# Kernel tuning notes

Measured on AMD Instinct MI355X. Metric: run time of the kernel, lower is better.

Reference implementation:

```python
import jax, jax.numpy as jnp
import numpy as np

B, L, E = 64, 256, 512
H = 1024          # hidden_size
N = 128           # memory_size
HS = 64           # head_size (memory width)
NH = 4            # NTM heads
OUT = 1024        # output_size
TNH = 4           # transformer nhead
IN_DIM = E + NH * HS          # 768
POD = H + NH * HS             # 1280


def ln(x, g, b, eps=1e-5):
    mu = x.mean(-1, keepdims=True)
    v = ((x - mu) ** 2).mean(-1, keepdims=True)
    return (x - mu) / jnp.sqrt(v + eps) * g + b


def setup_inputs() -> dict:
    key = jax.random.key(0)
    ks = iter(jax.random.split(key, 64))
    def w(shape, s=0.05):
        return jax.random.normal(next(ks), shape, jnp.float32) * s
    f32 = jnp.float32
    return dict(
        x_emb=jax.random.normal(next(ks), (B, L, E), f32),
        in_g=jnp.ones(IN_DIM, f32), in_b=jnp.zeros(IN_DIM, f32),
        W_ih=w((4 * H, IN_DIM)), W_hh=w((4 * H, H)),
        b_ih=jnp.zeros(4 * H, f32), b_hh=jnp.zeros(4 * H, f32),
        cn_g=jnp.ones(H, f32), cn_b=jnp.zeros(H, f32),
        W_rk=w((NH * HS, H)), b_rk=jnp.zeros(NH * HS, f32),
        W_wk=w((NH * HS, H)), b_wk=jnp.zeros(NH * HS, f32),
        W_ws=w((NH, H)), b_ws=jnp.zeros(NH, f32),
        W_ev=w((NH * HS, H)), b_ev=jnp.zeros(NH * HS, f32),
        attn_w=w((3 * HS, HS)), attn_b=jnp.zeros(3 * HS, f32),
        attn_ow=w((HS, HS)), attn_ob=jnp.zeros(HS, f32),
        l1_w=w((2 * HS, HS)), l1_b=jnp.zeros(2 * HS, f32),
        l2_w=w((HS, 2 * HS)), l2_b=jnp.zeros(HS, f32),
        tn1_g=jnp.ones(HS, f32), tn1_b=jnp.zeros(HS, f32),
        tn2_g=jnp.ones(HS, f32), tn2_b=jnp.zeros(HS, f32),
        rkn_g=jnp.ones(HS, f32), rkn_b=jnp.zeros(HS, f32),
        wkn_g=jnp.ones(HS, f32), wkn_b=jnp.zeros(HS, f32),
        mn_g=jnp.ones(HS, f32), mn_b=jnp.zeros(HS, f32),
        po_g=jnp.ones(POD, f32), po_b=jnp.zeros(POD, f32),
        W_proj=w((OUT, POD)), b_proj=jnp.zeros(OUT, f32),
    )


def reference(x_emb, in_g, in_b, W_ih, W_hh, b_ih, b_hh, cn_g, cn_b,
              W_rk, b_rk, W_wk, b_wk, W_ws, b_ws, W_ev, b_ev,
              attn_w, attn_b, attn_ow, attn_ob, l1_w, l1_b, l2_w, l2_b,
              tn1_g, tn1_b, tn2_g, tn2_b, rkn_g, rkn_b, wkn_g, wkn_b,
              mn_g, mn_b, po_g, po_b, W_proj, b_proj):
    Bc = x_emb.shape[0]
    dh = HS // TNH

    def tblock(mem):  # [B, N, HS], eval-mode (dropout = identity)
        qkv = mem @ attn_w.T + attn_b
        q, k, v = jnp.split(qkv, 3, axis=-1)
        q = q.reshape(Bc, N, TNH, dh)
        k = k.reshape(Bc, N, TNH, dh)
        v = v.reshape(Bc, N, TNH, dh)
        a = jax.nn.softmax(jnp.einsum('bqhd,bkhd->bhqk', q, k) / jnp.sqrt(jnp.float32(dh)), axis=-1)
        o = jnp.einsum('bhqk,bkhd->bqhd', a, v).reshape(Bc, N, HS)
        o = o @ attn_ow.T + attn_ob
        x = ln(mem + o, tn1_g, tn1_b)
        ff = jax.nn.gelu(x @ l1_w.T + l1_b, approximate=False) @ l2_w.T + l2_b
        return ln(x + ff, tn2_g, tn2_b)

    def step(carry, x_t):
        h, c, mem, rc = carry
        inp = ln(jnp.concatenate([x_t, rc.reshape(Bc, -1)], axis=-1), in_g, in_b)
        gates = inp @ W_ih.T + b_ih + h @ W_hh.T + b_hh  # torch gate order i,f,g,o
        i, f, g, o = jnp.split(gates, 4, axis=-1)
        c = jax.nn.sigmoid(f) * c + jax.nn.sigmoid(i) * jnp.tanh(g)
        h = jax.nn.sigmoid(o) * jnp.tanh(c)
        hn = ln(h, cn_g, cn_b)
        rk = (hn @ W_rk.T + b_rk).reshape(Bc, NH, HS)
        wk = (hn @ W_wk.T + b_wk).reshape(Bc, NH, HS)
        ws = jax.nn.sigmoid(hn @ W_ws.T + b_ws)                    # [B, NH]
        ev = jax.nn.sigmoid(hn @ W_ev.T + b_ev).reshape(Bc, NH, HS)
        # addressing
        mem = tblock(mem)
        mem_n = ln(mem, mn_g, mn_b)
        rk = ln(rk, rkn_g, rkn_b)
        wk = ln(wk, wkn_g, wkn_b)
        rw = jax.nn.softmax(jnp.einsum('bnk,bmk->bnm', rk, mem_n), axis=-1)
        rc = jnp.einsum('bnm,bmh->bnh', rw, mem)
        ww = jax.nn.softmax(jnp.einsum('bnk,bmk->bnm', wk, mem_n), axis=-1)
        erase = jnp.einsum('bnm,bnh->bmh', ww, ev)
        mem = mem * (1.0 - erase)
        add = jnp.einsum('bnm,bnh->bmh', ww, ws[..., None] * wk)
        mem = mem + add
        out = ln(jnp.concatenate([hn, rc.reshape(Bc, -1)], axis=-1), po_g, po_b)
        logits = out @ W_proj.T + b_proj
        return (h, c, mem, rc), logits

    h0 = jnp.zeros((Bc, H), x_emb.dtype)
    c0 = jnp.zeros((Bc, H), x_emb.dtype)
    mem0 = jnp.zeros((Bc, N, HS), x_emb.dtype)
    rc0 = jnp.zeros((Bc, NH, HS), x_emb.dtype)
    (h, c, mem, _), outs = jax.lax.scan(step, (h0, c0, mem0, rc0), jnp.swapaxes(x_emb, 0, 1))
    return jnp.swapaxes(outs, 0, 1), mem, (h[None], c[None])
```

## Files before the change

### kernel.cpp

```cpp
#include <hip/hip_runtime.h>
#include <math.h>

typedef short s8v __attribute__((ext_vector_type(8)));
typedef float f32x4 __attribute__((ext_vector_type(4)));

__device__ inline float sigm(float x) { return 1.0f / (1.0f + expf(-x)); }
__device__ inline float dot4(const float4 a, const float4 b) {
  return a.x*b.x + a.y*b.y + a.z*b.z + a.w*b.w;
}
__device__ inline float wsum(float v) {
#pragma unroll
  for (int o = 32; o > 0; o >>= 1) v += __shfl_xor(v, o, 64);
  return v;
}
__device__ inline short f2bf(float f) {
  unsigned int u = __float_as_uint(f);
  unsigned int r = u + 0x7FFFu + ((u >> 16) & 1u);
  return (short)(r >> 16);
}
__device__ inline float bf2f(short h) {
  return __uint_as_float(((unsigned int)(unsigned short)h) << 16);
}
__device__ inline void storesplit(float v, short* __restrict__ hi,
                                  short* __restrict__ lo, size_t idx) {
  short h = f2bf(v);
  hi[idx] = h;
  lo[idx] = f2bf(v - bf2f(h));
}

template<int LD, int KS>
__device__ __forceinline__ void gemm4(const short* __restrict__ A,
                                      const short* __restrict__ B,
                                      f32x4 acc[4], int lane) {
  int off = (lane & 15) * LD + ((lane >> 4) * 8);
#pragma unroll 4
  for (int kb = 0; kb < KS; kb++) {
    int ko = off + kb*32;
    s8v bb = *(const s8v*)(B + ko);
#pragma unroll
    for (int m = 0; m < 4; m++) {
      s8v aa = *(const s8v*)(A + ko + m*16*LD);
      acc[m] = __builtin_amdgcn_mfma_f32_16x16x32_bf16(aa, bb, acc[m], 0,0,0);
    }
  }
}

__global__ void kprep_g(const float* __restrict__ Wih, const float* __restrict__ Whh,
                        short* __restrict__ WgH, short* __restrict__ WgL) {
  int r = blockIdx.y, k = blockIdx.x*256 + threadIdx.x;
  if (k < 1792) {
    int jt = r >> 6, rr = r & 63, ul = rr >> 2, gi = rr & 3;
    int orow = gi*1024 + jt*16 + ul;
    float v = (k < 768) ? Wih[(size_t)orow*768 + k] : Whh[(size_t)orow*1024 + (k-768)];
    storesplit(v, WgH, WgL, (size_t)r*1792 + k);
  }
}
__global__ void kprep_p(const float* __restrict__ Wp, short* __restrict__ W) {
  int j = blockIdx.y, k = blockIdx.x*256 + threadIdx.x;
  W[(size_t)j*1280 + k] = f2bf(Wp[(size_t)j*1280 + k]);
}
__global__ void kprep_h(const float* __restrict__ Wrk, const float* __restrict__ Wwk,
                        const float* __restrict__ Wev, const float* __restrict__ Wws,
                        short* __restrict__ WhH, short* __restrict__ WhL) {
  int j = blockIdx.y, k = blockIdx.x*256 + threadIdx.x;
  float v;
  if (j < 256)      v = Wrk[(size_t)j*1024 + k];
  else if (j < 512) v = Wwk[(size_t)(j-256)*1024 + k];
  else if (j < 768) v = Wev[(size_t)(j-512)*1024 + k];
  else if (j < 772) v = Wws[(size_t)(j-768)*1024 + k];
  else v = 0.f;
  storesplit(v, WhH, WhL, (size_t)j*1024 + k);
}
__global__ void kprep_q(const float* __restrict__ aw, short* __restrict__ WH,
                        short* __restrict__ WL) {
  int i = blockIdx.x*64 + threadIdx.x;
  storesplit(aw[i], WH, WL, i);
}

__global__ __launch_bounds__(256) void k_prep0(
    const float* __restrict__ x_emb, const float* __restrict__ in_g,
    const float* __restrict__ in_b, short* __restrict__ inbH,
    short* __restrict__ inbL)
{
  __shared__ float rs[4], rq[4];
  int b = blockIdx.x, tid = threadIdx.x, lane = tid & 63, wid = tid >> 6;
  float v3[3]; float s = 0.f, sq = 0.f;
#pragma unroll
  for (int i = 0; i < 3; i++) {
    int k = tid + i * 256;
    float v = (k < 512) ? x_emb[(size_t)b * 256 * 512 + k] : 0.f;
    v3[i] = v; s += v; sq += v * v;
  }
  s = wsum(s); sq = wsum(sq);
  if (lane == 0) { rs[wid] = s; rq[wid] = sq; }
  __syncthreads();
  float ts = rs[0]+rs[1]+rs[2]+rs[3], tq = rq[0]+rq[1]+rq[2]+rq[3];
  float mu = ts / 768.f, var = tq / 768.f - mu * mu;
  float rstd = rsqrtf(var + 1e-5f);
#pragma unroll
  for (int i = 0; i < 3; i++) {
    int k = tid + i * 256;
    storesplit((v3[i] - mu) * rstd * in_g[k] + in_b[k], inbH, inbL, b*1792 + k);
  }
}

__global__ __launch_bounds__(512) void kAB(
    const short* __restrict__ inbH, const short* __restrict__ inbL,
    short* __restrict__ inbHn, short* __restrict__ inbLn,
    const short* __restrict__ WgH, const short* __restrict__ WgL,
    const float* __restrict__ b_ih, const float* __restrict__ b_hh,
    float* __restrict__ cbuf, float* __restrict__ hbuf,
    float* __restrict__ hstat, unsigned* __restrict__ gctr,
    const short* __restrict__ membH, const short* __restrict__ membL,
    const short* __restrict__ WqH, const short* __restrict__ WqL,
    const float* __restrict__ attn_b,
    float* __restrict__ mem,
    const float* __restrict__ attn_ow, const float* __restrict__ attn_ob,
    const float* __restrict__ l1w, const float* __restrict__ l1b,
    const float* __restrict__ l2w, const float* __restrict__ l2b,
    const float* __restrict__ tn1g, const float* __restrict__ tn1b,
    const float* __restrict__ tn2g, const float* __restrict__ tn2b,
    const float* __restrict__ cn_g, const float* __restrict__ cn_b,
    const short* __restrict__ WhH, const short* __restrict__ WhL,
    float* __restrict__ hp,
    const short* __restrict__ pob16, const short* __restrict__ Wp16,
    const float* __restrict__ b_proj, float* __restrict__ outs, int t)
{
  __shared__ float pool[35200];
  int bid = blockIdx.x, tid = threadIdx.x, lane = tid & 63;
  if (bid < 64) {
    if (t >= 256) return;
    int jt = bid;
    int kt = tid >> 8;
    int tl = tid & 255;
    int w4 = (tid >> 6) & 3;
    short (*sT)[4][2560] = (short(*)[4][2560])((char*)pool + kt*40960);
    int k0 = kt * 896;
    int srow = tl >> 2, scol = (tl & 3) * 8;
    const short* gAH = inbH + srow*1792 + k0 + scol;
    const short* gAL = inbL + srow*1792 + k0 + scol;
    const short* gBH = WgH + (size_t)(jt*64 + srow)*1792 + k0 + scol;
    const short* gBL = WgL + (size_t)(jt*64 + srow)*1792 + k0 + scol;
    int4 rAH = *(const int4*)gAH, rAL = *(const int4*)gAL;
    int4 rBH = *(const int4*)gBH, rBL = *(const int4*)gBL;
    *(int4*)&sT[0][0][srow*40 + scol] = rAH;
    *(int4*)&sT[0][1][srow*40 + scol] = rAL;
    *(int4*)&sT[0][2][srow*40 + scol] = rBH;
    *(int4*)&sT[0][3][srow*40 + scol] = rBL;
    f32x4 acc[4] = {};
    int arow = lane & 15, akk = (lane >> 4) * 8;
    for (int c = 0; c < 28; ++c) {
      int cur = c & 1;
      if (c < 27) {
        rAH = *(const int4*)(gAH + (c+1)*32);
        rAL = *(const int4*)(gAL + (c+1)*32);
        rBH = *(const int4*)(gBH + (c+1)*32);
        rBL = *(const int4*)(gBL + (c+1)*32);
      }
      __syncthreads();
      s8v bh = *(const s8v*)&sT[cur][2][(w4*16 + arow)*40 + akk];
      s8v bl = *(const s8v*)&sT[cur][3][(w4*16 + arow)*40 + akk];
#pragma unroll
      for (int ms = 0; ms < 4; ++ms) {
        s8v ah = *(const s8v*)&sT[cur][0][(arow + ms*16)*40 + akk];
        s8v al = *(const s8v*)&sT[cur][1][(arow + ms*16)*40 + akk];
        acc[ms] = __builtin_amdgcn_mfma_f32_16x16x32_bf16(ah, bh, acc[ms], 0,0,0);
        acc[ms] = __builtin_amdgcn_mfma_f32_16x16x32_bf16(al, bh, acc[ms], 0,0,0);
        acc[ms] = __builtin_amdgcn_mfma_f32_16x16x32_bf16(ah, bl, acc[ms], 0,0,0);
      }
      if (c < 27) {
        *(int4*)&sT[cur^1][0][srow*40 + scol] = rAH;
        *(int4*)&sT[cur^1][1][srow*40 + scol] = rAL;
        *(int4*)&sT[cur^1][2][srow*40 + scol] = rBH;
        *(int4*)&sT[cur^1][3][srow*40 + scol] = rBL;
      }
    }
    __syncthreads();
    float* sC = pool;
    float* sRed = pool + 8704;
    {
      float* sCk = sC + kt*4352;
      int rr = w4*16 + (lane & 15);
#pragma unroll
      for (int ms = 0; ms < 4; ms++)
#pragma unroll
        for (int r = 0; r < 4; r++) {
          int b = ms*16 + (lane>>4)*4 + r;
          sCk[b*68 + rr] = acc[ms][r];
        }
    }
    __syncthreads();
    {
      int b = tid & 63, ug = tid >> 6;
      float sh = 0.f, sh2 = 0.f;
#pragma unroll
      for (int q = 0; q < 2; q++) {
        int ul = ug*2 + q;
        int u = jt*16 + ul;
        float gi_ = sC[b*68 + ul*4 + 0] + sC[4352 + b*68 + ul*4 + 0] + b_ih[u]        + b_hh[u];
        float gf  = sC[b*68 + ul*4 + 1] + sC[4352 + b*68 + ul*4 + 1] + b_ih[1024 + u] + b_hh[1024 + u];
        float gg  = sC[b*68 + ul*4 + 2] + sC[4352 + b*68 + ul*4 + 2] + b_ih[2048 + u] + b_hh[2048 + u];
        float go  = sC[b*68 + ul*4 + 3] + sC[4352 + b*68 + ul*4 + 3] + b_ih[3072 + u] + b_hh[3072 + u];
        float cn = sigm(gf)*cbuf[b*1024 + u] + sigm(gi_)*tanhf(gg);
        float hh = sigm(go)*tanhf(cn);
        cbuf[b*1024 + u] = cn;
        hbuf[b*1024 + u] = hh;
        storesplit(hh, inbHn, inbLn, b*1792 + 768 + u);
        sh += hh; sh2 += hh*hh;
      }
      sRed[ug*64 + b] = sh;
      sRed[512 + ug*64 + b] = sh2;
    }
    __syncthreads();
    if (tid < 64) {
      float s0 = 0.f, s1 = 0.f;
#pragma unroll
      for (int p = 0; p < 8; p++) { s0 += sRed[p*64 + tid]; s1 += sRed[512 + p*64 + tid]; }
      hstat[(tid*64 + jt)*2]     = s0;
      hstat[(tid*64 + jt)*2 + 1] = s1;
    }
    __syncthreads();
    if (tid == 0) {
      __threadfence();
      __hip_atomic_fetch_add(gctr, 1u, __ATOMIC_RELEASE, __HIP_MEMORY_SCOPE_AGENT);
    }
  } else if (bid < 320) {
    if (t >= 256) return;
    float* sK  = pool;
    float* sV  = pool + 8704;
    float* sX  = pool + 17408;
    float* sM  = pool + 19584;
    float* sO  = pool + 21760;
    float* sS  = pool + 23936;
    float* sRed= pool + 34176;
    int pb = bid - 64;
    int b = pb & 63, mt = pb >> 6;
    int m0 = mt * 32;
    int wid = tid >> 6;
    {
      const short* Ah = membH + (size_t)b * 8192;
      const short* Al = membL + (size_t)b * 8192;
      int ao = (wid*16 + (lane & 15)) * 64 + (lane >> 4) * 8;
      s8v ah0 = *(const s8v*)(Ah + ao);
      s8v ah1 = *(const s8v*)(Ah + ao + 32);
      s8v al0 = *(const s8v*)(Al + ao);
      s8v al1 = *(const s8v*)(Al + ao + 32);
      int bo = (lane & 15) * 64 + (lane >> 4) * 8;
      for (int n = 0; n < 12; n++) {
        s8v bh0 = *(const s8v*)(WqH + bo + n*1024);
        s8v bh1 = *(const s8v*)(WqH + bo + n*1024 + 32);
        s8v bl0 = *(const s8v*)(WqL + bo + n*1024);
        s8v bl1 = *(const s8v*)(WqL + bo + n*1024 + 32);
        f32x4 acc = {};
        acc = __builtin_amdgcn_mfma_f32_16x16x32_bf16(ah0, bh0, acc, 0,0,0);
        acc = __builtin_amdgcn_mfma_f32_16x16x32_bf16(ah1, bh1, acc, 0,0,0);
        acc = __builtin_amdgcn_mfma_f32_16x16x32_bf16(al0, bh0, acc, 0,0,0);
        acc = __builtin_amdgcn_mfma_f32_16x16x32_bf16(al1, bh1, acc, 0,0,0);
        acc = __builtin_amdgcn_mfma_f32_16x16x32_bf16(ah0, bl0, acc, 0,0,0);
        acc = __builtin_amdgcn_mfma_f32_16x16x32_bf16(ah1, bl1, acc, 0,0,0);
        int j = n*16 + (lane & 15);
        int ch = j >> 6, jj = j & 63;
        float bv = attn_b[j];
#pragma unroll
        for (int r = 0; r < 4; r++) {
          int mr = wid*16 + (lane>>4)*4 + r;
          float v = acc[r] + bv;
          if (ch == 0) {
            if (mr >= m0 && mr < m0 + 32) sX[(mr - m0)*68 + jj] = v;
          } else if (ch == 1) sK[mr*64 + jj] = v;
          else sV[mr*64 + jj] = v;
        }
      }
    }
    {
      int i = tid*4;
      int m = i >> 6, s = i & 63;
      *(float4*)&sM[m*68+s] = *(const float4*)&mem[(size_t)b*8192 + m0*64 + i];
    }
    __syncthreads();
    int m = tid >> 4, hd = (tid >> 2) & 3, q = tid & 3;
    const float* qp = sX + m*68 + hd*16;
    float4 q0 = *(const float4*)(qp),   q1 = *(const float4*)(qp+4);
    float4 q2 = *(const float4*)(qp+8), q3 = *(const float4*)(qp+12);
    int kmb = q * 32;
    float mx = -1e30f;
#pragma unroll 4
    for (int kk = 0; kk < 32; kk++) {
      const float* kp = sK + (kmb+kk)*64 + hd*16;
      float sc = dot4(q0, *(const float4*)kp)     + dot4(q1, *(const float4*)(kp+4))
               + dot4(q2, *(const float4*)(kp+8)) + dot4(q3, *(const float4*)(kp+12));
      mx = fmaxf(mx, sc * 0.25f);
    }
    float4 o0 = {0,0,0,0}, o1 = {0,0,0,0}, o2 = {0,0,0,0}, o3 = {0,0,0,0};
    float sum = 0.f;
#pragma unroll 4
    for (int kk = 0; kk < 32; kk++) {
      const float* kp = sK + (kmb+kk)*64 + hd*16;
      float sc = dot4(q0, *(const float4*)kp)     + dot4(q1, *(const float4*)(kp+4))
               + dot4(q2, *(const float4*)(kp+8)) + dot4(q3, *(const float4*)(kp+12));
      float e = expf(sc * 0.25f - mx);
      sum += e;
      const float* vp = sV + (kmb+kk)*64 + hd*16;
      float4 v0 = *(const float4*)vp,     v1 = *(const float4*)(vp+4);
      float4 v2 = *(const float4*)(vp+8), v3 = *(const float4*)(vp+12);
      o0.x += e*v0.x; o0.y += e*v0.y; o0.z += e*v0.z; o0.w += e*v0.w;
      o1.x += e*v1.x; o1.y += e*v1.y; o1.z += e*v1.z; o1.w += e*v1.w;
      o2.x += e*v2.x; o2.y += e*v2.y; o2.z += e*v2.z; o2.w += e*v2.w;
      o3.x += e*v3.x; o3.y += e*v3.y; o3.z += e*v3.z; o3.w += e*v3.w;
    }
    {
      float* pp = sS + tid*20;
      *(float4*)&pp[0]  = o0; *(float4*)&pp[4]  = o1;
      *(float4*)&pp[8]  = o2; *(float4*)&pp[12] = o3;
      sRed[tid] = mx; sRed[512+tid] = sum;
    }
    __syncthreads();
    if (q == 0) {
      float m1 = sRed[tid+1], m2 = sRed[tid+2], m3 = sRed[tid+3];
      float M = fmaxf(fmaxf(mx, m1), fmaxf(m2, m3));
      float e0 = expf(mx - M), e1 = expf(m1 - M), e2 = expf(m2 - M), e3 = expf(m3 - M);
      float inv = 1.0f / (sum*e0 + sRed[512+tid+1]*e1 + sRed[512+tid+2]*e2
                          + sRed[512+tid+3]*e3);
      const float* p1 = sS + (tid+1)*20;
      const float* p2 = sS + (tid+2)*20;
      const float* p3 = sS + (tid+3)*20;
      float oo[16];
      *(float4*)&oo[0] = o0; *(float4*)&oo[4] = o1;
      *(float4*)&oo[8] = o2; *(float4*)&oo[12] = o3;
      float* op = sO + m*68 + hd*16;
#pragma unroll
      for (int d = 0; d < 16; d++)
        op[d] = (oo[d]*e0 + p1[d]*e1 + p2[d]*e2 + p3[d]*e3) * inv;
    }
    __syncthreads();
    for (int idx = tid; idx < 4096; idx += 512) {
      int j = idx >> 6, s = idx & 63;
      sS[j*68 + s] = attn_ow[idx];
    }
    __syncthreads();
    {
      int mm = tid >> 4, jset = tid & 15;
      float4 orow[16];
#pragma unroll
      for (int r = 0; r < 16; r++) orow[r] = *(const float4*)&sO[mm*68 + r*4];
#pragma unroll
      for (int i = 0; i < 4; i++) {
        int j = jset + 16*i;
        const float* wr = sS + j*68;
        float acc = attn_ob[j];
#pragma unroll
        for (int r = 0; r < 16; r++) acc += dot4(orow[r], *(const float4*)&wr[r*4]);
        sM[mm*68 + j] += acc;
      }
    }
    __syncthreads();
    for (int r = wid; r < 32; r += 8) {
      float v = sM[r*68 + lane];
      float ssum = wsum(v), ssq = wsum(v*v);
      float mu = ssum*(1.f/64), var = ssq*(1.f/64) - mu*mu;
      sX[r*68+lane] = (v - mu)*rsqrtf(var+1e-5f)*tn1g[lane] + tn1b[lane];
    }
    for (int idx = tid; idx < 8192; idx += 512) {
      int f = idx >> 6, s = idx & 63;
      sK[f*68 + s] = l1w[idx];
    }
    for (int idx = tid; idx < 8192; idx += 512) {
      int j = idx >> 7, s = idx & 127;
      sV[j*132 + s] = l2w[idx];
    }
    __syncthreads();
    {
      int mm = tid >> 4, fs = tid & 15;
      float4 xr[16];
#pragma unroll
      for (int r = 0; r < 16; r++) xr[r] = *(const float4*)&sX[mm*68 + r*4];
#pragma unroll 4
      for (int i = 0; i < 8; i++) {
        int f = fs + 16*i;
        const float* wr = sK + f*68;
        float acc = l1b[f];
#pragma unroll
        for (int r = 0; r < 16; r++) acc += dot4(xr[r], *(const float4*)&wr[r*4]);
        sS[mm*132 + f] = 0.5f*acc*(1.0f + erff(acc*0.70710678118654752f));
      }
    }
    __syncthreads();
    {
      int mm = tid >> 4, jset = tid & 15;
      float acc6[4];
#pragma unroll
      for (int i = 0; i < 4; i++) acc6[i] = sX[mm*68 + jset + 16*i] + l2b[jset + 16*i];
#pragma unroll
      for (int h = 0; h < 2; h++) {
        float4 fr[16];
#pragma unroll
        for (int r = 0; r < 16; r++) fr[r] = *(const float4*)&sS[mm*132 + h*64 + r*4];
#pragma unroll
        for (int i = 0; i < 4; i++) {
          int j = jset + 16*i;
          const float* wr = sV + j*132 + h*64;
          float a = 0.f;
#pragma unroll
          for (int r = 0; r < 16; r++) a += dot4(fr[r], *(const float4*)&wr[r*4]);
          acc6[i] += a;
        }
      }
#pragma unroll
      for (int i = 0; i < 4; i++) sO[mm*68 + jset + 16*i] = acc6[i];
    }
    __syncthreads();
    for (int r = wid; r < 32; r += 8) {
      float v = sO[r*68 + lane];
      float ssum = wsum(v), ssq = wsum(v*v);
      float mu = ssum*(1.f/64), var = ssq*(1.f/64) - mu*mu;
      mem[(size_t)b*8192 + (m0+r)*64 + lane] =
          (v - mu)*rsqrtf(var+1e-5f)*tn2g[lane] + tn2b[lane];
    }
  } else if (bid < 328) {
    if (t == 0) return;
    int jt = bid - 320;
    int w = tid >> 6;
    f32x4 acc[4] = {};
    const short* B = Wp16 + (size_t)(jt*128 + w*16) * 1280;
    gemm4<1280, 40>(pob16, B, acc, lane);
    int j = jt*128 + w*16 + (lane & 15);
    float bv = b_proj[j];
#pragma unroll
    for (int ms = 0; ms < 4; ms++)
#pragma unroll
      for (int r = 0; r < 4; r++) {
        int b = ms*16 + (lane>>4)*4 + r;
        outs[((size_t)b*256 + (t-1))*1024 + j] = acc[ms][r] + bv;
      }
  } else {
    if (t >= 256) return;
    int wid = tid >> 6;
    if (tid == 0) {
      unsigned target = 64u * (unsigned)(t + 1);
      while (__hip_atomic_load(gctr, __ATOMIC_ACQUIRE, __HIP_MEMORY_SCOPE_AGENT) < target)
        __builtin_amdgcn_s_sleep(2);
    }
    __syncthreads();
    int hb = bid - 328;
    int kt = hb & 3, jt = hb >> 2;
    {
      int b2 = tid & 63, part = tid >> 6;
      float s0 = 0.f, s1 = 0.f;
#pragma unroll 4
      for (int m2 = 0; m2 < 8; m2++) {
        int jt2 = part*8 + m2;
        s0 += hstat[(b2*64 + jt2)*2];
        s1 += hstat[(b2*64 + jt2)*2 + 1];
      }
      pool[part*64 + b2] = s0;
      pool[512 + part*64 + b2] = s1;
    }
    __syncthreads();
    if (tid < 64) {
      float ts = 0.f, tq = 0.f;
#pragma unroll
      for (int p2 = 0; p2 < 8; p2++) {
        ts += pool[p2*64 + tid];
        tq += pool[512 + p2*64 + tid];
      }
      float mu = ts / 1024.f;
      pool[1024+tid] = mu;
      pool[1088+tid] = rsqrtf(tq/1024.f - mu*mu + 1e-5f);
    }
    __syncthreads();
    short* sAH = (short*)&pool[1152];
    short* sAL = sAH + 2560;
    int srow = tid >> 3, scol = (tid & 7) * 4;
    int arow = lane & 15, akk = (lane >> 4) * 8;
    f32x4 acc[4] = {};
    for (int c = 0; c < 8; ++c) {
      __syncthreads();
      {
        float mu = pool[1024 + srow], rsd = pool[1088 + srow];
        int kbase = kt*256 + c*32 + scol;
        const float* hpt = hbuf + srow*1024 + kbase;
#pragma unroll
        for (int i = 0; i < 4; i++) {
          float hnv = (hpt[i] - mu) * rsd * cn_g[kbase + i] + cn_b[kbase + i];
          short hh = f2bf(hnv);
          sAH[srow*40 + scol + i] = hh;
          sAL[srow*40 + scol + i] = f2bf(hnv - bf2f(hh));
        }
      }
      __syncthreads();
      if (wid < 4) {
        size_t bo = (size_t)(jt*64 + wid*16 + arow)*1024 + kt*256 + c*32 + akk;
        s8v bh = *(const s8v*)(WhH + bo);
        s8v bl = *(const s8v*)(WhL + bo);
#pragma unroll
        for (int ms = 0; ms < 4; ++ms) {
          s8v ah = *(const s8v*)&sAH[(arow + ms*16)*40 + akk];
          s8v al = *(const s8v*)&sAL[(arow + ms*16)*40 + akk];
          acc[ms] = __builtin_amdgcn_mfma_f32_16x16x32_bf16(ah, bh, acc[ms], 0,0,0);
          acc[ms] = __builtin_amdgcn_mfma_f32_16x16x32_bf16(al, bh, acc[ms], 0,0,0);
          acc[ms] = __builtin_amdgcn_mfma_f32_16x16x32_bf16(ah, bl, acc[ms], 0,0,0);
        }
      }
    }
    if (wid < 4) {
      int j = jt*64 + wid*16 + (lane & 15);
#pragma unroll
      for (int ms = 0; ms < 4; ms++)
#pragma unroll
        for (int r = 0; r < 4; r++) {
          int b2 = ms*16 + (lane>>4)*4 + r;
          hp[(size_t)kt*53248 + b2*832 + j] = acc[ms][r];
        }
    }
  }
}

__global__ __launch_bounds__(512) void kC(
    float* __restrict__ mem, short* __restrict__ membH, short* __restrict__ membL,
    const float* __restrict__ hp, const float* __restrict__ hstat,
    const float* __restrict__ hbuf,
    const float* __restrict__ b_rk, const float* __restrict__ b_wk,
    const float* __restrict__ b_ev, const float* __restrict__ b_ws,
    const float* __restrict__ rkn_g, const float* __restrict__ rkn_b,
    const float* __restrict__ wkn_g, const float* __restrict__ wkn_b,
    const float* __restrict__ cn_g, const float* __restrict__ cn_b,
    const float* __restrict__ mng, const float* __restrict__ mnb,
    const float* __restrict__ pog, const float* __restrict__ pob,
    const float* __restrict__ x_emb, const float* __restrict__ in_g,
    const float* __restrict__ in_b,
    short* __restrict__ inbHn, short* __restrict__ inbLn,
    short* __restrict__ pob16, int tnext)
{
  __shared__ float P[20960];
  float* sMT  = P;
  float* sMN  = P + 8192;
  float* sHn  = P + 16512;
  float* sRk  = P + 17536;
  float* sWk  = P + 17792;
  float* sEv  = P + 18048;
  float* sWs  = P + 18304;
  float* sRw  = P + 18308;
  float* sWw  = P + 18820;
  float* sRc  = P + 19332;
  float* sRcP = P + 19588;
  float* rs   = P + 20100;
  float* rq   = P + 20108;
  float* sHst = P + 20116;
  int b = blockIdx.x, tid = threadIdx.x, lane = tid & 63, wv = tid >> 6;
  for (int i = tid*4; i < 8192; i += 2048)
    *(float4*)&sMT[i] = *(const float4*)&mem[(size_t)b*8192 + i];
  if (wv == 0) {
    float v0 = hstat[(b*64 + lane)*2], v1 = hstat[(b*64 + lane)*2 + 1];
    float s0 = wsum(v0), s1 = wsum(v1);
    if (lane == 0) {
      float mu = s0 / 1024.f;
      sHst[0] = mu;
      sHst[1] = rsqrtf(s1/1024.f - mu*mu + 1e-5f);
    }
  }
  __syncthreads();
  {
    float mu = sHst[0], rstd = sHst[1];
    for (int u = tid; u < 1024; u += 512)
      sHn[u] = (hbuf[b*1024 + u] - mu)*rstd*cn_g[u] + cn_b[u];
  }
  {
    const float* h0 = hp + (size_t)b*832;
    const float* h1 = hp + 53248 + (size_t)b*832;
    const float* h2 = hp + 2*53248 + (size_t)b*832;
    const float* h3 = hp + 3*53248 + (size_t)b*832;
    if (wv < 4) {
      int idx = wv*64 + lane;
      float v = h0[idx] + h1[idx] + h2[idx] + h3[idx] + b_rk[idx];
      float ssum = wsum(v), ssq = wsum(v*v);
      float mu = ssum*(1.f/64), var = ssq*(1.f/64) - mu*mu;
      sRk[idx] = (v - mu)*rsqrtf(var+1e-5f)*rkn_g[lane] + rkn_b[lane];
    } else {
      int idx = (wv-4)*64 + lane;
      float v = h0[256+idx] + h1[256+idx] + h2[256+idx] + h3[256+idx] + b_wk[idx];
      float ssum = wsum(v), ssq = wsum(v*v);
      float mu = ssum*(1.f/64), var = ssq*(1.f/64) - mu*mu;
      sWk[idx] = (v - mu)*rsqrtf(var+1e-5f)*wkn_g[lane] + wkn_b[lane];
    }
    if (tid < 256)
      sEv[tid] = sigm(h0[512+tid] + h1[512+tid] + h2[512+tid] + h3[512+tid] + b_ev[tid]);
    if (tid >= 256 && tid < 260) {
      int n = tid - 256;
      sWs[n] = sigm(h0[768+n] + h1[768+n] + h2[768+n] + h3[768+n] + b_ws[n]);
    }
  }
  for (int r = wv; r < 128; r += 8) {
    float v = sMT[r*64 + lane];
    float ssum = wsum(v), ssq = wsum(v*v);
    float mu = ssum*(1.f/64), var = ssq*(1.f/64) - mu*mu;
    sMN[r*65 + lane] = (v - mu)*rsqrtf(var+1e-5f)*mng[lane] + mnb[lane];
  }
  __syncthreads();
#pragma unroll
  for (int q = 0; q < 2; q++) {
    int idx = tid + q*512;
    int which = idx >> 9;
    int n = (idx >> 7) & 3, m = idx & 127;
    const float* key = (which ? sWk : sRk) + n*64;
    const float* mr = sMN + m*65;
    float acc = 0.f;
#pragma unroll 8
    for (int k = 0; k < 64; k++) acc += key[k]*mr[k];
    (which ? sWw : sRw)[n*128 + m] = acc;
  }
  __syncthreads();
  {
    float* row = (wv < 4) ? (sRw + wv*128) : (sWw + (wv-4)*128);
    float a0 = row[lane], a1 = row[lane+64];
    float mx = fmaxf(a0, a1);
#pragma unroll
    for (int o = 32; o > 0; o >>= 1) mx = fmaxf(mx, __shfl_xor(mx, o, 64));
    float e0 = expf(a0 - mx), e1 = expf(a1 - mx);
    float inv = 1.0f / wsum(e0 + e1);
    row[lane] = e0*inv; row[lane+64] = e1*inv;
  }
  __syncthreads();
  {
    int idx = tid & 255, h2 = tid >> 8;
    int n = idx >> 6, s2 = idx & 63;
    float acc = 0.f;
    for (int mm = h2*64; mm < h2*64 + 64; mm++) acc += sRw[n*128 + mm] * sMT[mm*64 + s2];
    sRcP[tid] = acc;
  }
  __syncthreads();
  if (tid < 256) sRc[tid] = sRcP[tid] + sRcP[256 + tid];
  for (int idx = tid; idx < 8192; idx += 512) {
    int mm = idx >> 6, s2 = idx & 63;
    float er = 0.f, ad = 0.f;
#pragma unroll
    for (int n = 0; n < 4; n++) {
      float w = sWw[n*128 + mm];
      er += w * sEv[n*64 + s2];
      ad += w * sWs[n] * sWk[n*64 + s2];
    }
    float val = sMT[idx]*(1.0f - er) + ad;
    mem[(size_t)b*8192 + idx] = val;
    storesplit(val, membH, membL, (size_t)b*8192 + idx);
  }
  __syncthreads();
  {
    float v5[3]; float s = 0.f, sq = 0.f;
#pragma unroll
    for (int i = 0; i < 3; i++) {
      int k = tid + i*512;
      float v = 0.f;
      if (k < 1280) v = (k < 1024) ? sHn[k] : sRc[k-1024];
      v5[i] = v; s += v; sq += v*v;
    }
    s = wsum(s); sq = wsum(sq);
    if (lane == 0) { rs[wv] = s; rq[wv] = sq; }
    __syncthreads();
    float ts = 0.f, tq = 0.f;
#pragma unroll
    for (int p = 0; p < 8; p++) { ts += rs[p]; tq += rq[p]; }
    float mu = ts/1280.f, var = tq/1280.f - mu*mu;
    float rstd = rsqrtf(var + 1e-5f);
#pragma unroll
    for (int i = 0; i < 3; i++) {
      int k = tid + i*512;
      if (k < 1280) pob16[b*1280 + k] = f2bf((v5[i] - mu)*rstd*pog[k] + pob[k]);
    }
  }
  if (tnext < 256) {
    __syncthreads();
    float v3[2]; float s2 = 0.f, q2 = 0.f;
#pragma unroll
    for (int i = 0; i < 2; i++) {
      int k = tid + i*512;
      float v = 0.f;
      if (k < 768) v = (k < 512) ? x_emb[((size_t)b*256 + tnext)*512 + k] : sRc[k-512];
      v3[i] = v; s2 += v; q2 += v*v;
    }
    s2 = wsum(s2); q2 = wsum(q2);
    if (lane == 0) { rs[wv] = s2; rq[wv] = q2; }
    __syncthreads();
    float ts = 0.f, tq = 0.f;
#pragma unroll
    for (int p = 0; p < 8; p++) { ts += rs[p]; tq += rq[p]; }
    float mu = ts/768.f, var = tq/768.f - mu*mu;
    float rstd = rsqrtf(var + 1e-5f);
#pragma unroll
    for (int i = 0; i < 2; i++) {
      int k = tid + i*512;
      if (k < 768)
        storesplit((v3[i] - mu)*rstd*in_g[k] + in_b[k], inbHn, inbLn, b*1792 + k);
    }
  }
}

__global__ void k_final(const float* __restrict__ mem, const float* __restrict__ hbuf,
                        const float* __restrict__ cbuf, float* __restrict__ out)
{
  int i = blockIdx.x * 256 + threadIdx.x;
  if (i < 524288) out[16777216 + i] = mem[i];
  if (i < 65536) {
    out[17301504 + i] = hbuf[i];
    out[17367040 + i] = cbuf[i];
  }
}

extern "C" void kernel_launch(void* const* d_in, const int* in_sizes, int n_in,
                              void* d_out, int out_size, void* d_ws, size_t ws_size,
                              hipStream_t stream) {
  const float* x_emb  = (const float*)d_in[0];
  const float* in_g   = (const float*)d_in[1];
  const float* in_b   = (const float*)d_in[2];
  const float* W_ih   = (const float*)d_in[3];
  const float* W_hh   = (const float*)d_in[4];
  const float* b_ih   = (const float*)d_in[5];
  const float* b_hh   = (const float*)d_in[6];
  const float* cn_g   = (const float*)d_in[7];
  const float* cn_b   = (const float*)d_in[8];
  const float* W_rk   = (const float*)d_in[9];
  const float* b_rk   = (const float*)d_in[10];
  const float* W_wk   = (const float*)d_in[11];
  const float* b_wk   = (const float*)d_in[12];
  const float* W_ws   = (const float*)d_in[13];
  const float* b_ws   = (const float*)d_in[14];
  const float* W_ev   = (const float*)d_in[15];
  const float* b_ev   = (const float*)d_in[16];
  const float* attn_w = (const float*)d_in[17];
  const float* attn_b = (const float*)d_in[18];
  const float* attn_ow= (const float*)d_in[19];
  const float* attn_ob= (const float*)d_in[20];
  const float* l1_w   = (const float*)d_in[21];
  const float* l1_b   = (const float*)d_in[22];
  const float* l2_w   = (const float*)d_in[23];
  const float* l2_b   = (const float*)d_in[24];
  const float* tn1_g  = (const float*)d_in[25];
  const float* tn1_b  = (const float*)d_in[26];
  const float* tn2_g  = (const float*)d_in[27];
  const float* tn2_b  = (const float*)d_in[28];
  const float* rkn_g  = (const float*)d_in[29];
  const float* rkn_b  = (const float*)d_in[30];
  const float* wkn_g  = (const float*)d_in[31];
  const float* wkn_b  = (const float*)d_in[32];
  const float* mn_g   = (const float*)d_in[33];
  const float* mn_b   = (const float*)d_in[34];
  const float* po_g   = (const float*)d_in[35];
  const float* po_b   = (const float*)d_in[36];
  const float* W_proj = (const float*)d_in[37];
  const float* b_proj = (const float*)d_in[38];

  float* ws = (float*)d_ws;
  float* mem   = ws;
  float* cbuf  = ws + 524288;
  float* hbuf  = ws + 589824;
  float* hstat = ws + 655360;
  float* hp    = ws + 663552;
  unsigned* gctr = (unsigned*)(ws + 876544);
  short* sb    = (short*)(ws + 876560);
  short* inbH0 = sb;
  short* inbL0 = sb + 114688;
  short* inbH1 = sb + 229376;
  short* inbL1 = sb + 344064;
  short* membH = sb + 458752;
  short* membL = sb + 983040;
  short* pob16 = sb + 1507328;
  short* WqH   = sb + 1589248;
  short* WqL   = sb + 1601536;
  short* WgH   = sb + 1613824;
  short* WgL   = sb + 8953856;
  short* WhH   = sb + 16293888;
  short* WhL   = sb + 17145856;
  short* Wp16  = sb + 17997824;

  hipMemsetAsync(ws, 0, 655360 * sizeof(float), stream);
  hipMemsetAsync(gctr, 0, 64, stream);
  hipMemsetAsync(sb, 0, 1507328 * sizeof(short), stream);

  kprep_g<<<dim3(7, 4096), 256, 0, stream>>>(W_ih, W_hh, WgH, WgL);
  kprep_p<<<dim3(5, 1024), 256, 0, stream>>>(W_proj, Wp16);
  kprep_h<<<dim3(4, 832), 256, 0, stream>>>(W_rk, W_wk, W_ev, W_ws, WhH, WhL);
  kprep_q<<<dim3(192), 64, 0, stream>>>(attn_w, WqH, WqL);
  k_prep0<<<64, 256, 0, stream>>>(x_emb, in_g, in_b, inbH0, inbL0);

  float* outs = (float*)d_out;
  short* bufsH[2] = {inbH0, inbH1};
  short* bufsL[2] = {inbL0, inbL1};
  for (int t = 0; t < 256; t++) {
    kAB<<<380, 512, 0, stream>>>(bufsH[t&1], bufsL[t&1], bufsH[(t+1)&1], bufsL[(t+1)&1],
                                 WgH, WgL, b_ih, b_hh, cbuf, hbuf, hstat, gctr,
                                 membH, membL, WqH, WqL, attn_b, mem,
                                 attn_ow, attn_ob, l1_w, l1_b, l2_w, l2_b,
                                 tn1_g, tn1_b, tn2_g, tn2_b, cn_g, cn_b,
                                 WhH, WhL, hp, pob16, Wp16, b_proj, outs, t);
    kC<<<64, 512, 0, stream>>>(mem, membH, membL, hp, hstat, hbuf,
                               b_rk, b_wk, b_ev, b_ws,
                               rkn_g, rkn_b, wkn_g, wkn_b, cn_g, cn_b,
                               mn_g, mn_b, po_g, po_b,
                               x_emb, in_g, in_b,
                               bufsH[(t+1)&1], bufsL[(t+1)&1], pob16, t+1);
  }
  kAB<<<380, 512, 0, stream>>>(bufsH[0], bufsL[0], bufsH[1], bufsL[1],
                               WgH, WgL, b_ih, b_hh, cbuf, hbuf, hstat, gctr,
                               membH, membL, WqH, WqL, attn_b, mem,
                               attn_ow, attn_ob, l1_w, l1_b, l2_w, l2_b,
                               tn1_g, tn1_b, tn2_g, tn2_b, cn_g, cn_b,
                               WhH, WhL, hp, pob16, Wp16, b_proj, outs, 256);
  k_final<<<2048, 256, 0, stream>>>(mem, hbuf, cbuf, (float*)d_out);
}
```

Before: 29.75 ms.

## Compute QKV once per batch in kC and halve transformer block count

Moves the memory QKV projection (MFMA on a split-bf16 copy of memory) from the per-tile transformer blocks in kAB into kC, right after the memory update. The result is stored as fp32 in a new global qkv buffer, so each batch computes it once instead of four times. kAB's transformer part now uses 128 blocks that each loop over two 32-row tiles and load K/V/Q from the buffer, cutting the grid from 380 to 252 blocks. This removes redundant projection work and the membH/membL round trip, but adds serial MFMA work to kC's 64 blocks and halves parallelism in the transformer phase.

```diff
diff --git a/kernel.cpp b/kernel.cpp
--- a/kernel.cpp
+++ b/kernel.cpp
@@ -104,6 +104,16 @@
   }
 }
 
+__global__ __launch_bounds__(256) void k_prepq0(
+    const float* __restrict__ attn_b, float* __restrict__ qkv)
+{
+  int b = blockIdx.x, tid = threadIdx.x;
+  for (int i = tid; i < 24576; i += 256) {
+    int ch = i >> 13, j = i & 63;
+    qkv[(size_t)b*24576 + i] = attn_b[ch*64 + j];
+  }
+}
+
 __global__ __launch_bounds__(512) void kAB(
     const short* __restrict__ inbH, const short* __restrict__ inbL,
     short* __restrict__ inbHn, short* __restrict__ inbLn,
@@ -111,10 +121,7 @@
     const float* __restrict__ b_ih, const float* __restrict__ b_hh,
     float* __restrict__ cbuf, float* __restrict__ hbuf,
     float* __restrict__ hstat, unsigned* __restrict__ gctr,
-    const short* __restrict__ membH, const short* __restrict__ membL,
-    const short* __restrict__ WqH, const short* __restrict__ WqL,
-    const float* __restrict__ attn_b,
-    float* __restrict__ mem,
+    const float* __restrict__ qkv, float* __restrict__ mem,
     const float* __restrict__ attn_ow, const float* __restrict__ attn_ob,
     const float* __restrict__ l1w, const float* __restrict__ l1b,
     const float* __restrict__ l2w, const float* __restrict__ l2b,
@@ -224,7 +231,7 @@
       __threadfence();
       __hip_atomic_fetch_add(gctr, 1u, __ATOMIC_RELEASE, __HIP_MEMORY_SCOPE_AGENT);
     }
-  } else if (bid < 320) {
+  } else if (bid < 192) {
     if (t >= 256) return;
     float* sK  = pool;
     float* sV  = pool + 8704;
@@ -234,191 +241,165 @@
     float* sS  = pool + 23936;
     float* sRed= pool + 34176;
     int pb = bid - 64;
-    int b = pb & 63, mt = pb >> 6;
-    int m0 = mt * 32;
+    int b = pb & 63, pr = pb >> 6;
     int wid = tid >> 6;
-    {
-      const short* Ah = membH + (size_t)b * 8192;
-      const short* Al = membL + (size_t)b * 8192;
-      int ao = (wid*16 + (lane & 15)) * 64 + (lane >> 4) * 8;
-      s8v ah0 = *(const s8v*)(Ah + ao);
-      s8v ah1 = *(const s8v*)(Ah + ao + 32);
-      s8v al0 = *(const s8v*)(Al + ao);
-      s8v al1 = *(const s8v*)(Al + ao + 32);
-      int bo = (lane & 15) * 64 + (lane >> 4) * 8;
-      for (int n = 0; n < 12; n++) {
-        s8v bh0 = *(const s8v*)(WqH + bo + n*1024);
-        s8v bh1 = *(const s8v*)(WqH + bo + n*1024 + 32);
-        s8v bl0 = *(const s8v*)(WqL + bo + n*1024);
-        s8v bl1 = *(const s8v*)(WqL + bo + n*1024 + 32);
-        f32x4 acc = {};
-        acc = __builtin_amdgcn_mfma_f32_16x16x32_bf16(ah0, bh0, acc, 0,0,0);
-        acc = __builtin_amdgcn_mfma_f32_16x16x32_bf16(ah1, bh1, acc, 0,0,0);
-        acc = __builtin_amdgcn_mfma_f32_16x16x32_bf16(al0, bh0, acc, 0,0,0);
-        acc = __builtin_amdgcn_mfma_f32_16x16x32_bf16(al1, bh1, acc, 0,0,0);
-        acc = __builtin_amdgcn_mfma_f32_16x16x32_bf16(ah0, bl0, acc, 0,0,0);
-        acc = __builtin_amdgcn_mfma_f32_16x16x32_bf16(ah1, bl1, acc, 0,0,0);
-        int j = n*16 + (lane & 15);
-        int ch = j >> 6, jj = j & 63;
-        float bv = attn_b[j];
-#pragma unroll
-        for (int r = 0; r < 4; r++) {
-          int mr = wid*16 + (lane>>4)*4 + r;
-          float v = acc[r] + bv;
-          if (ch == 0) {
-            if (mr >= m0 && mr < m0 + 32) sX[(mr - m0)*68 + jj] = v;
-          } else if (ch == 1) sK[mr*64 + jj] = v;
-          else sV[mr*64 + jj] = v;
-        }
-      }
-    }
-    {
-      int i = tid*4;
-      int m = i >> 6, s = i & 63;
-      *(float4*)&sM[m*68+s] = *(const float4*)&mem[(size_t)b*8192 + m0*64 + i];
-    }
-    __syncthreads();
-    int m = tid >> 4, hd = (tid >> 2) & 3, q = tid & 3;
-    const float* qp = sX + m*68 + hd*16;
-    float4 q0 = *(const float4*)(qp),   q1 = *(const float4*)(qp+4);
-    float4 q2 = *(const float4*)(qp+8), q3 = *(const float4*)(qp+12);
-    int kmb = q * 32;
-    float mx = -1e30f;
+    const float* qb = qkv + (size_t)b*3*8192;
+    for (int it = 0; it < 2; ++it) {
+      int m0 = (pr*2 + it) * 32;
+      for (int i = tid*4; i < 8192; i += 2048) {
+        *(float4*)&sK[i] = *(const float4*)&qb[8192 + i];
+        *(float4*)&sV[i] = *(const float4*)&qb[16384 + i];
+      }
+      {
+        int i = tid*4;
+        int m = i >> 6, s = i & 63;
+        *(float4*)&sX[m*68+s] = *(const float4*)&qb[m0*64 + i];
+        *(float4*)&sM[m*68+s] = *(const float4*)&mem[(size_t)b*8192 + m0*64 + i];
+      }
+      __syncthreads();
+      int m = tid >> 4, hd = (tid >> 2) & 3, q = tid & 3;
+      const float* qp = sX + m*68 + hd*16;
+      float4 q0 = *(const float4*)(qp),   q1 = *(const float4*)(qp+4);
+      float4 q2 = *(const float4*)(qp+8), q3 = *(const float4*)(qp+12);
+      int kmb = q * 32;
+      float mx = -1e30f;
 #pragma unroll 4
-    for (int kk = 0; kk < 32; kk++) {
-      const float* kp = sK + (kmb+kk)*64 + hd*16;
-      float sc = dot4(q0, *(const float4*)kp)     + dot4(q1, *(const float4*)(kp+4))
-               + dot4(q2, *(const float4*)(kp+8)) + dot4(q3, *(const float4*)(kp+12));
-      mx = fmaxf(mx, sc * 0.25f);
-    }
-    float4 o0 = {0,0,0,0}, o1 = {0,0,0,0}, o2 = {0,0,0,0}, o3 = {0,0,0,0};
-    float sum = 0.f;
+      for (int kk = 0; kk < 32; kk++) {
+        const float* kp = sK + (kmb+kk)*64 + hd*16;
+        float sc = dot4(q0, *(const float4*)kp)     + dot4(q1, *(const float4*)(kp+4))
+                 + dot4(q2, *(const float4*)(kp+8)) + dot4(q3, *(const float4*)(kp+12));
+        mx = fmaxf(mx, sc * 0.25f);
+      }
+      float4 o0 = {0,0,0,0}, o1 = {0,0,0,0}, o2 = {0,0,0,0}, o3 = {0,0,0,0};
+      float sum = 0.f;
 #pragma unroll 4
-    for (int kk = 0; kk < 32; kk++) {
-      const float* kp = sK + (kmb+kk)*64 + hd*16;
-      float sc = dot4(q0, *(const float4*)kp)     + dot4(q1, *(const float4*)(kp+4))
-               + dot4(q2, *(const float4*)(kp+8)) + dot4(q3, *(const float4*)(kp+12));
-      float e = expf(sc * 0.25f - mx);
-      sum += e;
-      const float* vp = sV + (kmb+kk)*64 + hd*16;
-      float4 v0 = *(const float4*)vp,     v1 = *(const float4*)(vp+4);
-      float4 v2 = *(const float4*)(vp+8), v3 = *(const float4*)(vp+12);
-      o0.x += e*v0.x; o0.y += e*v0.y; o0.z += e*v0.z; o0.w += e*v0.w;
-      o1.x += e*v1.x; o1.y += e*v1.y; o1.z += e*v1.z; o1.w += e*v1.w;
-      o2.x += e*v2.x; o2.y += e*v2.y; o2.z += e*v2.z; o2.w += e*v2.w;
-      o3.x += e*v3.x; o3.y += e*v3.y; o3.z += e*v3.z; o3.w += e*v3.w;
-    }
-    {
-      float* pp = sS + tid*20;
-      *(float4*)&pp[0]  = o0; *(float4*)&pp[4]  = o1;
-      *(float4*)&pp[8]  = o2; *(float4*)&pp[12] = o3;
-      sRed[tid] = mx; sRed[512+tid] = sum;
-    }
-    __syncthreads();
-    if (q == 0) {
-      float m1 = sRed[tid+1], m2 = sRed[tid+2], m3 = sRed[tid+3];
-      float M = fmaxf(fmaxf(mx, m1), fmaxf(m2, m3));
-      float e0 = expf(mx - M), e1 = expf(m1 - M), e2 = expf(m2 - M), e3 = expf(m3 - M);
-      float inv = 1.0f / (sum*e0 + sRed[512+tid+1]*e1 + sRed[512+tid+2]*e2
-                          + sRed[512+tid+3]*e3);
-      const float* p1 = sS + (tid+1)*20;
-      const float* p2 = sS + (tid+2)*20;
-      const float* p3 = sS + (tid+3)*20;
-      float oo[16];
-      *(float4*)&oo[0] = o0; *(float4*)&oo[4] = o1;
-      *(float4*)&oo[8] = o2; *(float4*)&oo[12] = o3;
-      float* op = sO + m*68 + hd*16;
-#pragma unroll
-      for (int d = 0; d < 16; d++)
-        op[d] = (oo[d]*e0 + p1[d]*e1 + p2[d]*e2 + p3[d]*e3) * inv;
-    }
-    __syncthreads();
-    for (int idx = tid; idx < 4096; idx += 512) {
-      int j = idx >> 6, s = idx & 63;
-      sS[j*68 + s] = attn_ow[idx];
-    }
-    __syncthreads();
-    {
-      int mm = tid >> 4, jset = tid & 15;
-      float4 orow[16];
-#pragma unroll
-      for (int r = 0; r < 16; r++) orow[r] = *(const float4*)&sO[mm*68 + r*4];
-#pragma unroll
-      for (int i = 0; i < 4; i++) {
-        int j = jset + 16*i;
-        const float* wr = sS + j*68;
-        float acc = attn_ob[j];
-#pragma unroll
-        for (int r = 0; r < 16; r++) acc += dot4(orow[r], *(const float4*)&wr[r*4]);
-        sM[mm*68 + j] += acc;
-      }
-    }
-    __syncthreads();
-    for (int r = wid; r < 32; r += 8) {
-      float v = sM[r*68 + lane];
-      float ssum = wsum(v), ssq = wsum(v*v);
-      float mu = ssum*(1.f/64), var = ssq*(1.f/64) - mu*mu;
-      sX[r*68+lane] = (v - mu)*rsqrtf(var+1e-5f)*tn1g[lane] + tn1b[lane];
-    }
-    for (int idx = tid; idx < 8192; idx += 512) {
-      int f = idx >> 6, s = idx & 63;
-      sK[f*68 + s] = l1w[idx];
-    }
-    for (int idx = tid; idx < 8192; idx += 512) {
-      int j = idx >> 7, s = idx & 127;
-      sV[j*132 + s] = l2w[idx];
-    }
-    __syncthreads();
-    {
-      int mm = tid >> 4, fs = tid & 15;
-      float4 xr[16];
-#pragma unroll
-      for (int r = 0; r < 16; r++) xr[r] = *(const float4*)&sX[mm*68 + r*4];
-#pragma unroll 4
-      for (int i = 0; i < 8; i++) {
-        int f = fs + 16*i;
-        const float* wr = sK + f*68;
-        float acc = l1b[f];
-#pragma unroll
-        for (int r = 0; r < 16; r++) acc += dot4(xr[r], *(const float4*)&wr[r*4]);
-        sS[mm*132 + f] = 0.5f*acc*(1.0f + erff(acc*0.70710678118654752f));
-      }
-    }
-    __syncthreads();
-    {
-      int mm = tid >> 4, jset = tid & 15;
-      float acc6[4];
-#pragma unroll
-      for (int i = 0; i < 4; i++) acc6[i] = sX[mm*68 + jset + 16*i] + l2b[jset + 16*i];
-#pragma unroll
-      for (int h = 0; h < 2; h++) {
-        float4 fr[16];
-#pragma unroll
-        for (int r = 0; r < 16; r++) fr[r] = *(const float4*)&sS[mm*132 + h*64 + r*4];
+      for (int kk = 0; kk < 32; kk++) {
+        const float* kp = sK + (kmb+kk)*64 + hd*16;
+        float sc = dot4(q0, *(const float4*)kp)     + dot4(q1, *(const float4*)(kp+4))
+                 + dot4(q2, *(const float4*)(kp+8)) + dot4(q3, *(const float4*)(kp+12));
+        float e = expf(sc * 0.25f - mx);
+        sum += e;
+        const float* vp = sV + (kmb+kk)*64 + hd*16;
+        float4 v0 = *(const float4*)vp,     v1 = *(const float4*)(vp+4);
+        float4 v2 = *(const float4*)(vp+8), v3 = *(const float4*)(vp+12);
+        o0.x += e*v0.x; o0.y += e*v0.y; o0.z += e*v0.z; o0.w += e*v0.w;
+        o1.x += e*v1.x; o1.y += e*v1.y; o1.z += e*v1.z; o1.w += e*v1.w;
+        o2.x += e*v2.x; o2.y += e*v2.y; o2.z += e*v2.z; o2.w += e*v2.w;
+        o3.x += e*v3.x; o3.y += e*v3.y; o3.z += e*v3.z; o3.w += e*v3.w;
+      }
+      {
+        float* pp = sS + tid*20;
+        *(float4*)&pp[0]  = o0; *(float4*)&pp[4]  = o1;
+        *(float4*)&pp[8]  = o2; *(float4*)&pp[12] = o3;
+        sRed[tid] = mx; sRed[512+tid] = sum;
+      }
+      __syncthreads();
+      if (q == 0) {
+        float m1 = sRed[tid+1], m2 = sRed[tid+2], m3 = sRed[tid+3];
+        float M = fmaxf(fmaxf(mx, m1), fmaxf(m2, m3));
+        float e0 = expf(mx - M), e1 = expf(m1 - M), e2 = expf(m2 - M), e3 = expf(m3 - M);
+        float inv = 1.0f / (sum*e0 + sRed[512+tid+1]*e1 + sRed[512+tid+2]*e2
+                            + sRed[512+tid+3]*e3);
+        const float* p1 = sS + (tid+1)*20;
+        const float* p2 = sS + (tid+2)*20;
+        const float* p3 = sS + (tid+3)*20;
+        float oo[16];
+        *(float4*)&oo[0] = o0; *(float4*)&oo[4] = o1;
+        *(float4*)&oo[8] = o2; *(float4*)&oo[12] = o3;
+        float* op = sO + m*68 + hd*16;
+#pragma unroll
+        for (int d = 0; d < 16; d++)
+          op[d] = (oo[d]*e0 + p1[d]*e1 + p2[d]*e2 + p3[d]*e3) * inv;
+      }
+      __syncthreads();
+      for (int idx = tid; idx < 4096; idx += 512) {
+        int j = idx >> 6, s = idx & 63;
+        sS[j*68 + s] = attn_ow[idx];
+      }
+      __syncthreads();
+      {
+        int mm = tid >> 4, jset = tid & 15;
+        float4 orow[16];
+#pragma unroll
+        for (int r = 0; r < 16; r++) orow[r] = *(const float4*)&sO[mm*68 + r*4];
 #pragma unroll
         for (int i = 0; i < 4; i++) {
           int j = jset + 16*i;
-          const float* wr = sV + j*132 + h*64;
-          float a = 0.f;
-#pragma unroll
-          for (int r = 0; r < 16; r++) a += dot4(fr[r], *(const float4*)&wr[r*4]);
-          acc6[i] += a;
+          const float* wr = sS + j*68;
+          float acc = attn_ob[j];
+#pragma unroll
+          for (int r = 0; r < 16; r++) acc += dot4(orow[r], *(const float4*)&wr[r*4]);
+          sM[mm*68 + j] += acc;
         }
       }
-#pragma unroll
-      for (int i = 0; i < 4; i++) sO[mm*68 + jset + 16*i] = acc6[i];
-    }
-    __syncthreads();
-    for (int r = wid; r < 32; r += 8) {
-      float v = sO[r*68 + lane];
-      float ssum = wsum(v), ssq = wsum(v*v);
-      float mu = ssum*(1.f/64), var = ssq*(1.f/64) - mu*mu;
-      mem[(size_t)b*8192 + (m0+r)*64 + lane] =
-          (v - mu)*rsqrtf(var+1e-5f)*tn2g[lane] + tn2b[lane];
-    }
-  } else if (bid < 328) {
+      __syncthreads();
+      for (int r = wid; r < 32; r += 8) {
+        float v = sM[r*68 + lane];
+        float ssum = wsum(v), ssq = wsum(v*v);
+        float mu = ssum*(1.f/64), var = ssq*(1.f/64) - mu*mu;
+        sX[r*68+lane] = (v - mu)*rsqrtf(var+1e-5f)*tn1g[lane] + tn1b[lane];
+      }
+      for (int idx = tid; idx < 8192; idx += 512) {
+        int f = idx >> 6, s = idx & 63;
+        sK[f*68 + s] = l1w[idx];
+      }
+      for (int idx = tid; idx < 8192; idx += 512) {
+        int j = idx >> 7, s = idx & 127;
+        sV[j*132 + s] = l2w[idx];
+      }
+      __syncthreads();
+      {
+        int mm = tid >> 4, fs = tid & 15;
+        float4 xr[16];
+#pragma unroll
+        for (int r = 0; r < 16; r++) xr[r] = *(const float4*)&sX[mm*68 + r*4];
+#pragma unroll 4
+        for (int i = 0; i < 8; i++) {
+          int f = fs + 16*i;
+          const float* wr = sK + f*68;
+          float acc = l1b[f];
+#pragma unroll
+          for (int r = 0; r < 16; r++) acc += dot4(xr[r], *(const float4*)&wr[r*4]);
+          sS[mm*132 + f] = 0.5f*acc*(1.0f + erff(acc*0.70710678118654752f));
+        }
+      }
+      __syncthreads();
+      {
+        int mm = tid >> 4, jset = tid & 15;
+        float acc6[4];
+#pragma unroll
+        for (int i = 0; i < 4; i++) acc6[i] = sX[mm*68 + jset + 16*i] + l2b[jset + 16*i];
+#pragma unroll
+        for (int h = 0; h < 2; h++) {
+          float4 fr[16];
+#pragma unroll
+          for (int r = 0; r < 16; r++) fr[r] = *(const float4*)&sS[mm*132 + h*64 + r*4];
+#pragma unroll
+          for (int i = 0; i < 4; i++) {
+            int j = jset + 16*i;
+            const float* wr = sV + j*132 + h*64;
+            float a = 0.f;
+#pragma unroll
+            for (int r = 0; r < 16; r++) a += dot4(fr[r], *(const float4*)&wr[r*4]);
+            acc6[i] += a;
+          }
+        }
+#pragma unroll
+        for (int i = 0; i < 4; i++) sO[mm*68 + jset + 16*i] = acc6[i];
+      }
+      __syncthreads();
+      for (int r = wid; r < 32; r += 8) {
+        float v = sO[r*68 + lane];
+        float ssum = wsum(v), ssq = wsum(v*v);
+        float mu = ssum*(1.f/64), var = ssq*(1.f/64) - mu*mu;
+        mem[(size_t)b*8192 + (m0+r)*64 + lane] =
+            (v - mu)*rsqrtf(var+1e-5f)*tn2g[lane] + tn2b[lane];
+      }
+      __syncthreads();
+    }
+  } else if (bid < 200) {
     if (t == 0) return;
-    int jt = bid - 320;
+    int jt = bid - 192;
     int w = tid >> 6;
     f32x4 acc[4] = {};
     const short* B = Wp16 + (size_t)(jt*128 + w*16) * 1280;
@@ -441,7 +422,7 @@
         __builtin_amdgcn_s_sleep(2);
     }
     __syncthreads();
-    int hb = bid - 328;
+    int hb = bid - 200;
     int kt = hb & 3, jt = hb >> 2;
     {
       int b2 = tid & 63, part = tid >> 6;
@@ -516,7 +497,7 @@
 }
 
 __global__ __launch_bounds__(512) void kC(
-    float* __restrict__ mem, short* __restrict__ membH, short* __restrict__ membL,
+    float* __restrict__ mem,
     const float* __restrict__ hp, const float* __restrict__ hstat,
     const float* __restrict__ hbuf,
     const float* __restrict__ b_rk, const float* __restrict__ b_wk,
@@ -528,6 +509,8 @@
     const float* __restrict__ pog, const float* __restrict__ pob,
     const float* __restrict__ x_emb, const float* __restrict__ in_g,
     const float* __restrict__ in_b,
+    const short* __restrict__ WqH, const short* __restrict__ WqL,
+    const float* __restrict__ attn_b, float* __restrict__ qkv,
     short* __restrict__ inbHn, short* __restrict__ inbLn,
     short* __restrict__ pob16, int tnext)
 {
@@ -640,9 +623,47 @@
     }
     float val = sMT[idx]*(1.0f - er) + ad;
     mem[(size_t)b*8192 + idx] = val;
-    storesplit(val, membH, membL, (size_t)b*8192 + idx);
+    sMT[idx] = val;
   }
   __syncthreads();
+  short* sAH = (short*)(P + 8192);
+  short* sAL = sAH + 8192;
+  for (int idx = tid; idx < 8192; idx += 512) {
+    float v = sMT[idx];
+    short h = f2bf(v);
+    sAH[idx] = h;
+    sAL[idx] = f2bf(v - bf2f(h));
+  }
+  __syncthreads();
+  {
+    int ao = (wv*16 + (lane & 15))*64 + (lane >> 4)*8;
+    s8v ah0 = *(const s8v*)(sAH + ao);
+    s8v ah1 = *(const s8v*)(sAH + ao + 32);
+    s8v al0 = *(const s8v*)(sAL + ao);
+    s8v al1 = *(const s8v*)(sAL + ao + 32);
+    int bo = (lane & 15)*64 + (lane >> 4)*8;
+    for (int n = 0; n < 12; n++) {
+      s8v bh0 = *(const s8v*)(WqH + bo + n*1024);
+      s8v bh1 = *(const s8v*)(WqH + bo + n*1024 + 32);
+      s8v bl0 = *(const s8v*)(WqL + bo + n*1024);
+      s8v bl1 = *(const s8v*)(WqL + bo + n*1024 + 32);
+      f32x4 acc = {};
+      acc = __builtin_amdgcn_mfma_f32_16x16x32_bf16(ah0, bh0, acc, 0,0,0);
+      acc = __builtin_amdgcn_mfma_f32_16x16x32_bf16(ah1, bh1, acc, 0,0,0);
+      acc = __builtin_amdgcn_mfma_f32_16x16x32_bf16(al0, bh0, acc, 0,0,0);
+      acc = __builtin_amdgcn_mfma_f32_16x16x32_bf16(al1, bh1, acc, 0,0,0);
+      acc = __builtin_amdgcn_mfma_f32_16x16x32_bf16(ah0, bl0, acc, 0,0,0);
+      acc = __builtin_amdgcn_mfma_f32_16x16x32_bf16(ah1, bl1, acc, 0,0,0);
+      int j = n*16 + (lane & 15);
+      int ch = j >> 6, jj = j & 63;
+      float bv = attn_b[j];
+#pragma unroll
+      for (int r = 0; r < 4; r++) {
+        int m0 = wv*16 + (lane>>4)*4 + r;
+        qkv[((size_t)(b*3 + ch)*128 + m0)*64 + jj] = acc[r] + bv;
+      }
+    }
+  }
   {
     float v5[3]; float s = 0.f, sq = 0.f;
 #pragma unroll
@@ -754,52 +775,52 @@
   float* hstat = ws + 655360;
   float* hp    = ws + 663552;
   unsigned* gctr = (unsigned*)(ws + 876544);
-  short* sb    = (short*)(ws + 876560);
+  float* qkvb  = ws + 876560;
+  short* sb    = (short*)(ws + 2449424);
   short* inbH0 = sb;
   short* inbL0 = sb + 114688;
   short* inbH1 = sb + 229376;
   short* inbL1 = sb + 344064;
-  short* membH = sb + 458752;
-  short* membL = sb + 983040;
-  short* pob16 = sb + 1507328;
-  short* WqH   = sb + 1589248;
-  short* WqL   = sb + 1601536;
-  short* WgH   = sb + 1613824;
-  short* WgL   = sb + 8953856;
-  short* WhH   = sb + 16293888;
-  short* WhL   = sb + 17145856;
-  short* Wp16  = sb + 17997824;
+  short* pob16 = sb + 458752;
+  short* WqH   = sb + 540672;
+  short* WqL   = sb + 552960;
+  short* WgH   = sb + 565248;
+  short* WgL   = sb + 7905280;
+  short* WhH   = sb + 15245312;
+  short* WhL   = sb + 16097280;
+  short* Wp16  = sb + 16949248;
 
   hipMemsetAsync(ws, 0, 655360 * sizeof(float), stream);
   hipMemsetAsync(gctr, 0, 64, stream);
-  hipMemsetAsync(sb, 0, 1507328 * sizeof(short), stream);
+  hipMemsetAsync(sb, 0, 458752 * sizeof(short), stream);
 
   kprep_g<<<dim3(7, 4096), 256, 0, stream>>>(W_ih, W_hh, WgH, WgL);
   kprep_p<<<dim3(5, 1024), 256, 0, stream>>>(W_proj, Wp16);
   kprep_h<<<dim3(4, 832), 256, 0, stream>>>(W_rk, W_wk, W_ev, W_ws, WhH, WhL);
   kprep_q<<<dim3(192), 64, 0, stream>>>(attn_w, WqH, WqL);
   k_prep0<<<64, 256, 0, stream>>>(x_emb, in_g, in_b, inbH0, inbL0);
+  k_prepq0<<<64, 256, 0, stream>>>(attn_b, qkvb);
 
   float* outs = (float*)d_out;
   short* bufsH[2] = {inbH0, inbH1};
   short* bufsL[2] = {inbL0, inbL1};
   for (int t = 0; t < 256; t++) {
-    kAB<<<380, 512, 0, stream>>>(bufsH[t&1], bufsL[t&1], bufsH[(t+1)&1], bufsL[(t+1)&1],
+    kAB<<<252, 512, 0, stream>>>(bufsH[t&1], bufsL[t&1], bufsH[(t+1)&1], bufsL[(t+1)&1],
                                  WgH, WgL, b_ih, b_hh, cbuf, hbuf, hstat, gctr,
-                                 membH, membL, WqH, WqL, attn_b, mem,
+                                 qkvb, mem,
                                  attn_ow, attn_ob, l1_w, l1_b, l2_w, l2_b,
                                  tn1_g, tn1_b, tn2_g, tn2_b, cn_g, cn_b,
                                  WhH, WhL, hp, pob16, Wp16, b_proj, outs, t);
-    kC<<<64, 512, 0, stream>>>(mem, membH, membL, hp, hstat, hbuf,
+    kC<<<64, 512, 0, stream>>>(mem, hp, hstat, hbuf,
                                b_rk, b_wk, b_ev, b_ws,
                                rkn_g, rkn_b, wkn_g, wkn_b, cn_g, cn_b,
                                mn_g, mn_b, po_g, po_b,
-                               x_emb, in_g, in_b,
+                               x_emb, in_g, in_b, WqH, WqL, attn_b, qkvb,
                                bufsH[(t+1)&1], bufsL[(t+1)&1], pob16, t+1);
   }
-  kAB<<<380, 512, 0, stream>>>(bufsH[0], bufsL[0], bufsH[1], bufsL[1],
+  kAB<<<252, 512, 0, stream>>>(bufsH[0], bufsL[0], bufsH[1], bufsL[1],
                                WgH, WgL, b_ih, b_hh, cbuf, hbuf, hstat, gctr,
-                               membH, membL, WqH, WqL, attn_b, mem,
+                               qkvb, mem,
                                attn_ow, attn_ob, l1_w, l1_b, l2_w, l2_b,
                                tn1_g, tn1_b, tn2_g, tn2_b, cn_g, cn_b,
                                WhH, WhL, hp, pob16, Wp16, b_proj, outs, 256);
```

Result: slower. 40.48 ms (+36.1%).
